# Kernel tuning notes

Hardware: AMD Instinct MI355X
Metric: run time of the kernel (lower is better)

The kernel has to match this reference:

```python
import jax, jax.numpy as jnp
import numpy as np

NUM_EXPERTS = 64


def setup_inputs() -> dict:
    key = jax.random.key(0)
    k1, k2 = jax.random.split(key)
    x = jax.random.normal(k1, (4, 4096, 2048), dtype=jnp.float32)
    # nn.Linear default init scale ~ 1/sqrt(dim); exact init irrelevant for correctness
    gate_w = jax.random.normal(k2, (NUM_EXPERTS, 2048), dtype=jnp.float32) * (1.0 / np.sqrt(2048.0))
    expert_bias = jnp.zeros((NUM_EXPERTS,), dtype=jnp.float32)
    return {"x": x, "gate_w": gate_w, "expert_bias": expert_bias, "top_k": 8}


def reference(x, gate_w, expert_bias, top_k):
    # x: [B, S, D]; gate_w: [E, D]; expert_bias: [E]
    B, S, D = x.shape
    x_flat = x.reshape(-1, D)                                  # [T, D], T = B*S
    logits = jnp.einsum('td,ed->te', x_flat, gate_w) + expert_bias  # [T, E]
    top_k_logits, top_k_indices = jax.lax.top_k(logits, top_k)      # [T, K]
    top_k_weights = jax.nn.softmax(top_k_logits, axis=-1)           # [T, K]
    # training-mode load counting (scatter_add over expert ids)
    expert_counts = jax.ops.segment_sum(
        jnp.ones((B * S * top_k,), dtype=jnp.float32),
        top_k_indices.reshape(-1),
        num_segments=NUM_EXPERTS,
    )                                                               # [E]
    return top_k_indices, top_k_weights, expert_counts
```

## Files before the change

### kernel.cpp

```cpp
#include <hip/hip_runtime.h>
#include <math.h>

#define T_TOKENS 16384
#define D_DIM    2048
#define E_EXP    64
#define TOPK     8
#define NS       4
#define KC       32
#define NCH      (D_DIM / NS / KC)
#define TT       64

typedef __attribute__((ext_vector_type(8))) short bf16x8;
typedef __attribute__((ext_vector_type(4))) float f32x4;

__device__ __forceinline__ unsigned short bf16rne(float f) {
  unsigned u = __builtin_bit_cast(unsigned, f);
  unsigned r = u + 0x7fffu + ((u >> 16) & 1u);
  return (unsigned short)(r >> 16);
}
__device__ __forceinline__ float bf16f(unsigned short h) {
  return __builtin_bit_cast(float, (unsigned)h << 16);
}

__global__ __launch_bounds__(256) void convert_g_kernel(
    const float* __restrict__ gw, unsigned short* __restrict__ ph,
    unsigned short* __restrict__ pl, float* __restrict__ counts_zero)
{
  const int id = blockIdx.x * 256 + threadIdx.x;
  if (blockIdx.x == 0 && threadIdx.x < E_EXP) counts_zero[threadIdx.x] = 0.0f;

  const int e  = id & 63;
  const int kq = (id >> 6) & 3;
  const int c  = id >> 8;
  const float* gp = &gw[(size_t)e * D_DIM + c * 32 + kq * 8];
  float4 v0 = *(const float4*)&gp[0];
  float4 v1 = *(const float4*)&gp[4];
  const float xs[8] = {v0.x, v0.y, v0.z, v0.w, v1.x, v1.y, v1.z, v1.w};
  bf16x8 hi, lo;
  #pragma unroll
  for (int j = 0; j < 8; ++j) {
    unsigned short h = bf16rne(xs[j]);
    hi[j] = (short)h;
    lo[j] = (short)bf16rne(xs[j] - bf16f(h));
  }
  *(bf16x8*)&ph[(size_t)id * 8] = hi;
  *(bf16x8*)&pl[(size_t)id * 8] = lo;
}

__global__ __launch_bounds__(256, 4) void moe_logits_kernel(
    const float* __restrict__ x, const unsigned short* __restrict__ ph,
    const unsigned short* __restrict__ pl, float* __restrict__ part)
{
  const int tid  = threadIdx.x;
  const int wave = tid >> 6;
  const int lane = tid & 63;
  const int l15  = lane & 15;
  const int quad = lane >> 4;
  const int ks   = blockIdx.y;
  const int k0   = ks * (D_DIM / NS);
  const int tokw = blockIdx.x * TT + wave * 16;

  const float* xg = &x[(size_t)(tokw + l15) * D_DIM + k0 + quad * 8];

  const unsigned short* bh_p = &ph[(((size_t)(k0 >> 5) * 4 + quad) * 64 + l15) * 8];
  const unsigned short* bl_p = &pl[(((size_t)(k0 >> 5) * 4 + quad) * 64 + l15) * 8];

  f32x4 acc[4];
  #pragma unroll
  for (int et = 0; et < 4; ++et) acc[et] = (f32x4){0.f, 0.f, 0.f, 0.f};

  float4 p0 = *(const float4*)xg;
  float4 p1 = *(const float4*)(xg + 4);

  #pragma unroll 1
  for (int c = 0; c < NCH; ++c) {
    const unsigned short* ch = bh_p + (size_t)c * 2048;
    const unsigned short* cl = bl_p + (size_t)c * 2048;
    bf16x8 bh[4], bl[4];
    #pragma unroll
    for (int et = 0; et < 4; ++et) {
      bh[et] = *(const bf16x8*)&ch[et * 128];
      bl[et] = *(const bf16x8*)&cl[et * 128];
    }

    float4 n0 = {0.f, 0.f, 0.f, 0.f}, n1 = {0.f, 0.f, 0.f, 0.f};
    if (c + 1 < NCH) {
      n0 = *(const float4*)(xg + (c + 1) * KC);
      n1 = *(const float4*)(xg + (c + 1) * KC + 4);
    }

    const float xs[8] = {p0.x, p0.y, p0.z, p0.w, p1.x, p1.y, p1.z, p1.w};
    bf16x8 ah, al;
    #pragma unroll
    for (int j = 0; j < 8; ++j) {
      unsigned short h = bf16rne(xs[j]);
      ah[j] = (short)h;
      al[j] = (short)bf16rne(xs[j] - bf16f(h));
    }

    #pragma unroll
    for (int et = 0; et < 4; ++et) {
      acc[et] = __builtin_amdgcn_mfma_f32_16x16x32_bf16(ah, bh[et], acc[et], 0, 0, 0);
      acc[et] = __builtin_amdgcn_mfma_f32_16x16x32_bf16(al, bh[et], acc[et], 0, 0, 0);
      acc[et] = __builtin_amdgcn_mfma_f32_16x16x32_bf16(ah, bl[et], acc[et], 0, 0, 0);
    }

    p0 = n0; p1 = n1;
  }

  #pragma unroll
  for (int et = 0; et < 4; ++et) {
    #pragma unroll
    for (int r = 0; r < 4; ++r) {
      const size_t t = (size_t)tokw + quad * 4 + r;
      part[((size_t)ks * T_TOKENS + t) * E_EXP + et * 16 + l15] = acc[et][r];
    }
  }
}

__global__ __launch_bounds__(64) void topk_kernel(
    const float* __restrict__ part, const float* __restrict__ bias,
    float* __restrict__ out)
{
  __shared__ unsigned hist[E_EXP];
  const int tid = threadIdx.x;
  const int t = blockIdx.x * 64 + tid;
  hist[tid] = 0;
  __syncthreads();

  float l[E_EXP];
  #pragma unroll
  for (int j = 0; j < E_EXP / 4; ++j) {
    float4 b = *(const float4*)&bias[j * 4];
    l[4*j] = b.x; l[4*j+1] = b.y; l[4*j+2] = b.z; l[4*j+3] = b.w;
  }
  #pragma unroll 2
  for (int ks = 0; ks < NS; ++ks) {
    const float4* p = (const float4*)&part[((size_t)ks * T_TOKENS + t) * E_EXP];
    #pragma unroll
    for (int j = 0; j < E_EXP / 4; ++j) {
      float4 v = p[j];
      l[4*j] += v.x; l[4*j+1] += v.y; l[4*j+2] += v.z; l[4*j+3] += v.w;
    }
  }

  float tv[TOPK]; int tix[TOPK];
  unsigned long long used = 0ull;
  #pragma unroll
  for (int k = 0; k < TOPK; ++k) {
    float best = -INFINITY; int bi = 0;
    #pragma unroll
    for (int j = 0; j < E_EXP; ++j) {
      bool ok = (((used >> j) & 1ull) == 0ull) && (l[j] > best);
      best = ok ? l[j] : best;
      bi   = ok ? j : bi;
    }
    tv[k] = best; tix[k] = bi;
    used |= (1ull << bi);
  }

  float m = tv[0], s = 0.0f, w[TOPK];
  #pragma unroll
  for (int k = 0; k < TOPK; ++k) { w[k] = expf(tv[k] - m); s += w[k]; }
  float inv = 1.0f / s;

  #pragma unroll
  for (int k = 0; k < TOPK; ++k) {
    out[(size_t)t * TOPK + k] = (float)tix[k];
    out[(size_t)T_TOKENS * TOPK + (size_t)t * TOPK + k] = w[k] * inv;
  }

  #pragma unroll
  for (int k = 0; k < TOPK; ++k) atomicAdd(&hist[tix[k]], 1u);
  __syncthreads();
  atomicAdd(&out[2 * (size_t)T_TOKENS * TOPK + tid], (float)hist[tid]);
}

extern "C" void kernel_launch(void* const* d_in, const int* in_sizes, int n_in,
                              void* d_out, int out_size, void* d_ws, size_t ws_size,
                              hipStream_t stream) {
  const float* x    = (const float*)d_in[0];
  const float* gw   = (const float*)d_in[1];
  const float* bias = (const float*)d_in[2];
  float* out  = (float*)d_out;

  float* part = (float*)d_ws;
  const size_t part_elems = (size_t)NS * T_TOKENS * E_EXP;
  unsigned short* ph = (unsigned short*)((char*)d_ws + part_elems * sizeof(float));
  unsigned short* pl = ph + (size_t)E_EXP * D_DIM;

  convert_g_kernel<<<dim3(E_EXP * D_DIM / 8 / 256), dim3(256), 0, stream>>>(
      gw, ph, pl, out + 2 * (size_t)T_TOKENS * TOPK);
  moe_logits_kernel<<<dim3(T_TOKENS / TT, NS), dim3(256), 0, stream>>>(
      x, ph, pl, part);
  topk_kernel<<<dim3(T_TOKENS / 64), dim3(64), 0, stream>>>(part, bias, out);
}
```

Measured before the change: 233.7 us.

## Fuse logits GEMM and top-k routing into one kernel via LDS reduction

Merges the split-K logits kernel and the top-k kernel into one 1024-thread block. Each group of four waves handles one K-slice, and the partial logits are reduced through a padded shared-memory slab instead of a global partial buffer. This removes the global write and re-read of the partial logits and one kernel launch. In exchange each block uses about 68 KB of LDS, which limits resident blocks per CU. After the reduction only one wave per block does the top-k and softmax, leaving a serial tail.

```diff
diff --git a/kernel.cpp b/kernel.cpp
--- a/kernel.cpp
+++ b/kernel.cpp
@@ -9,6 +9,7 @@
 #define KC       32
 #define NCH      (D_DIM / NS / KC)
 #define TT       64
+#define TOKP     68
 
 typedef __attribute__((ext_vector_type(8))) short bf16x8;
 typedef __attribute__((ext_vector_type(4))) float f32x4;
@@ -47,18 +48,23 @@
   *(bf16x8*)&pl[(size_t)id * 8] = lo;
 }
 
-__global__ __launch_bounds__(256, 4) void moe_logits_kernel(
+__global__ __launch_bounds__(1024, 4) void moe_fused_kernel(
     const float* __restrict__ x, const unsigned short* __restrict__ ph,
-    const unsigned short* __restrict__ pl, float* __restrict__ part)
+    const unsigned short* __restrict__ pl, const float* __restrict__ bias,
+    float* __restrict__ out)
 {
+  __shared__ float slab[NS * E_EXP * TOKP];
+  __shared__ unsigned hist[E_EXP];
+
   const int tid  = threadIdx.x;
   const int wave = tid >> 6;
   const int lane = tid & 63;
   const int l15  = lane & 15;
   const int quad = lane >> 4;
-  const int ks   = blockIdx.y;
-  const int k0   = ks * (D_DIM / NS);
-  const int tokw = blockIdx.x * TT + wave * 16;
+  const int wg   = wave & 3;
+  const int wsl  = wave >> 2;
+  const int k0   = wsl * (D_DIM / NS);
+  const int tokw = blockIdx.x * TT + wg * 16;
 
   const float* xg = &x[(size_t)(tokw + l15) * D_DIM + k0 + quad * 8];
 
@@ -110,39 +116,32 @@
 
   #pragma unroll
   for (int et = 0; et < 4; ++et) {
-    #pragma unroll
-    for (int r = 0; r < 4; ++r) {
-      const size_t t = (size_t)tokw + quad * 4 + r;
-      part[((size_t)ks * T_TOKENS + t) * E_EXP + et * 16 + l15] = acc[et][r];
-    }
+    *(f32x4*)&slab[((size_t)(wsl * E_EXP + et * 16 + l15)) * TOKP + wg * 16 + quad * 4] = acc[et];
   }
-}
-
-__global__ __launch_bounds__(64) void topk_kernel(
-    const float* __restrict__ part, const float* __restrict__ bias,
-    float* __restrict__ out)
-{
-  __shared__ unsigned hist[E_EXP];
-  const int tid = threadIdx.x;
-  const int t = blockIdx.x * 64 + tid;
-  hist[tid] = 0;
+  if (tid < E_EXP) hist[tid] = 0;
   __syncthreads();
 
+  {
+    const int e  = tid >> 4;
+    const int t4 = (tid & 15) * 4;
+    f32x4 s0 = *(const f32x4*)&slab[(size_t)(0 * E_EXP + e) * TOKP + t4];
+    f32x4 s1 = *(const f32x4*)&slab[(size_t)(1 * E_EXP + e) * TOKP + t4];
+    f32x4 s2 = *(const f32x4*)&slab[(size_t)(2 * E_EXP + e) * TOKP + t4];
+    f32x4 s3 = *(const f32x4*)&slab[(size_t)(3 * E_EXP + e) * TOKP + t4];
+    const float b = bias[e];
+    f32x4 v;
+    #pragma unroll
+    for (int j = 0; j < 4; ++j) v[j] = (((b + s0[j]) + s1[j]) + s2[j]) + s3[j];
+    *(f32x4*)&slab[(size_t)(0 * E_EXP + e) * TOKP + t4] = v;
+  }
+  __syncthreads();
+
+  if (tid >= TT) return;
+
+  const int t = tid;
   float l[E_EXP];
   #pragma unroll
-  for (int j = 0; j < E_EXP / 4; ++j) {
-    float4 b = *(const float4*)&bias[j * 4];
-    l[4*j] = b.x; l[4*j+1] = b.y; l[4*j+2] = b.z; l[4*j+3] = b.w;
-  }
-  #pragma unroll 2
-  for (int ks = 0; ks < NS; ++ks) {
-    const float4* p = (const float4*)&part[((size_t)ks * T_TOKENS + t) * E_EXP];
-    #pragma unroll
-    for (int j = 0; j < E_EXP / 4; ++j) {
-      float4 v = p[j];
-      l[4*j] += v.x; l[4*j+1] += v.y; l[4*j+2] += v.z; l[4*j+3] += v.w;
-    }
-  }
+  for (int j = 0; j < E_EXP; ++j) l[j] = slab[(size_t)j * TOKP + t];
 
   float tv[TOPK]; int tix[TOPK];
   unsigned long long used = 0ull;
@@ -164,16 +163,17 @@
   for (int k = 0; k < TOPK; ++k) { w[k] = expf(tv[k] - m); s += w[k]; }
   float inv = 1.0f / s;
 
+  const size_t gt = (size_t)blockIdx.x * TT + t;
   #pragma unroll
   for (int k = 0; k < TOPK; ++k) {
-    out[(size_t)t * TOPK + k] = (float)tix[k];
-    out[(size_t)T_TOKENS * TOPK + (size_t)t * TOPK + k] = w[k] * inv;
+    out[gt * TOPK + k] = (float)tix[k];
+    out[(size_t)T_TOKENS * TOPK + gt * TOPK + k] = w[k] * inv;
   }
 
   #pragma unroll
   for (int k = 0; k < TOPK; ++k) atomicAdd(&hist[tix[k]], 1u);
-  __syncthreads();
-  atomicAdd(&out[2 * (size_t)T_TOKENS * TOPK + tid], (float)hist[tid]);
+  __threadfence_block();
+  atomicAdd(&out[2 * (size_t)T_TOKENS * TOPK + t], (float)hist[t]);
 }
 
 extern "C" void kernel_launch(void* const* d_in, const int* in_sizes, int n_in,
@@ -184,14 +184,11 @@
   const float* bias = (const float*)d_in[2];
   float* out  = (float*)d_out;
 
-  float* part = (float*)d_ws;
-  const size_t part_elems = (size_t)NS * T_TOKENS * E_EXP;
-  unsigned short* ph = (unsigned short*)((char*)d_ws + part_elems * sizeof(float));
+  unsigned short* ph = (unsigned short*)d_ws;
   unsigned short* pl = ph + (size_t)E_EXP * D_DIM;
 
   convert_g_kernel<<<dim3(E_EXP * D_DIM / 8 / 256), dim3(256), 0, stream>>>(
       gw, ph, pl, out + 2 * (size_t)T_TOKENS * TOPK);
-  moe_logits_kernel<<<dim3(T_TOKENS / TT, NS), dim3(256), 0, stream>>>(
-      x, ph, pl, part);
-  topk_kernel<<<dim3(T_TOKENS / 64), dim3(64), 0, stream>>>(part, bias, out);
+  moe_fused_kernel<<<dim3(T_TOKENS / TT), dim3(1024), 0, stream>>>(
+      x, ph, pl, bias, out);
 }
```

Measured after the change: 215.3 us. 7.9% less time.
